# Optimization experiments

Hardware: AMD Instinct MI355X
Metric: run time of the kernel (lower is better)

The kernel has to match this reference:

```python
import jax, jax.numpy as jnp
import numpy as np

B = 4096
INPUT_DIM = 512
MAX_DIM = 4096
ACTIVE = 2048
INIT_LEAK = 0.1
INIT_THRESH = 0.5


def setup_inputs() -> dict:
    key = jax.random.key(0)
    ks = jax.random.split(key, 6)
    inputs = jax.random.normal(ks[0], (B, INPUT_DIM), dtype=jnp.float32)
    state = jax.random.normal(ks[1], (B, MAX_DIM), dtype=jnp.float32)
    # pre-allocated weights at max dimension, stddev=0.1 (RandomNormal)
    W_res = 0.1 * jax.random.normal(ks[2], (MAX_DIM, MAX_DIM), dtype=jnp.float32)
    W_in = 0.1 * jax.random.normal(ks[3], (MAX_DIM, INPUT_DIM), dtype=jnp.float32)
    W_gate = 0.1 * jax.random.normal(ks[4], (3 * MAX_DIM, INPUT_DIM), dtype=jnp.float32)
    # logit(leak_rate) and inverse-softplus(spike_threshold) constant inits
    leak_param = jnp.full((MAX_DIM,), np.log(INIT_LEAK / (1.0 - INIT_LEAK)), dtype=jnp.float32)
    thresh_param = jnp.full((MAX_DIM,), np.log(np.exp(INIT_THRESH) - 1.0), dtype=jnp.float32)
    return {
        "inputs": inputs,
        "state": state,
        "W_res": W_res,
        "W_in": W_in,
        "W_gate": W_gate,
        "leak_param": leak_param,
        "thresh_param": thresh_param,
        "active_size": ACTIVE,
    }


def reference(inputs, state, W_res, W_in, W_gate, leak_param, thresh_param, active_size):
    A = int(active_size)
    prev = state[:, :A]                              # [B, A]
    leak = jax.nn.sigmoid(leak_param[:A])            # [A]
    thresh = jax.nn.softplus(thresh_param[:A])       # [A]
    input_part = inputs @ W_in[:A].T                 # [B, A]
    res_part = prev @ W_res[:A, :A]                  # [B, A]
    gates = jax.nn.sigmoid(inputs @ W_gate[:3 * A].T)  # [B, 3A]
    i_gate, f_gate, o_gate = jnp.split(gates, 3, axis=-1)
    s = (1.0 - leak) * (f_gate * prev) + leak * jnp.tanh(i_gate * (input_part + res_part))
    s = o_gate * s
    s = jnp.where(s > thresh, s - thresh, s)         # spike-and-reset
    pad = state.shape[1] - A
    return jnp.pad(s, ((0, 0), (0, pad)))            # [B, MAX_DIM]
```

## Files before the change

### kernel.cpp

```cpp
#include <hip/hip_runtime.h>
#include <math.h>

typedef _Float16 f16;
typedef _Float16 f16x8 __attribute__((ext_vector_type(8)));
typedef _Float16 f16x4v __attribute__((ext_vector_type(4)));
typedef float f32x4 __attribute__((ext_vector_type(4)));

#define SPLIT_SC  2048.0f
#define INV_SPLIT (1.0f / 2048.0f)

__device__ __forceinline__ float sigmoidf_(float x) { return 1.0f / (1.0f + expf(-x)); }

#define GLOAD(ldsptr, gptr)                                                              \
    __builtin_amdgcn_global_load_lds((const __attribute__((address_space(1))) void*)(gptr), \
                                     (__attribute__((address_space(3))) void*)(ldsptr), 16, 0, 0)


__global__ void ksplit(const float* __restrict__ src, f16* __restrict__ dh,
                       f16* __restrict__ dl, int nquads)
{
    int i = blockIdx.x * blockDim.x + threadIdx.x;
    if (i >= nquads) return;
    float4 v = *(const float4*)(src + (size_t)i * 4);
    f16 h0 = (f16)v.x, h1 = (f16)v.y, h2 = (f16)v.z, h3 = (f16)v.w;
    f16x4v hv = {h0, h1, h2, h3};
    f16x4v lv = {(f16)((v.x - (float)h0) * SPLIT_SC), (f16)((v.y - (float)h1) * SPLIT_SC),
                 (f16)((v.z - (float)h2) * SPLIT_SC), (f16)((v.w - (float)h3) * SPLIT_SC)};
    *(f16x4v*)(dh + (size_t)i * 4) = hv;
    *(f16x4v*)(dl + (size_t)i * 4) = lv;
}

__global__ void ksplit_state(const float* __restrict__ src, f16* __restrict__ dh,
                             f16* __restrict__ dl)
{
    int idx = blockIdx.x * blockDim.x + threadIdx.x;
    int r = idx >> 9, c = (idx & 511) * 4;
    float4 v = *(const float4*)(src + (size_t)r * 4096 + c);
    f16 h0 = (f16)v.x, h1 = (f16)v.y, h2 = (f16)v.z, h3 = (f16)v.w;
    f16x4v hv = {h0, h1, h2, h3};
    f16x4v lv = {(f16)((v.x - (float)h0) * SPLIT_SC), (f16)((v.y - (float)h1) * SPLIT_SC),
                 (f16)((v.z - (float)h2) * SPLIT_SC), (f16)((v.w - (float)h3) * SPLIT_SC)};
    *(f16x4v*)(dh + (size_t)r * 2048 + c) = hv;
    *(f16x4v*)(dl + (size_t)r * 2048 + c) = lv;
}

__global__ void ktrsplit(const float* __restrict__ src, f16* __restrict__ th_,
                         f16* __restrict__ tl_)
{
    __shared__ float tile[32][33];
    const int tx = threadIdx.x & 31, ty = threadIdx.x >> 5;
    const int n0 = blockIdx.x * 32, k0 = blockIdx.y * 32;
    #pragma unroll
    for (int i = 0; i < 4; ++i)
        tile[ty + 8 * i][tx] = src[(size_t)(k0 + ty + 8 * i) * 4096 + n0 + tx];
    __syncthreads();
    #pragma unroll
    for (int i = 0; i < 4; ++i) {
        const int nl = ty + 8 * i;
        const float v = tile[tx][nl];
        const f16 h = (f16)v;
        const f16 l = (f16)((v - (float)h) * SPLIT_SC);
        const size_t o = (size_t)(n0 + nl) * 2048 + k0 + tx;
        th_[o] = h;
        tl_[o] = l;
    }
}

__global__ __launch_bounds__(256, 2)
void kgemm_res(const f16* __restrict__ Ah, const f16* __restrict__ Al,
               const f16* __restrict__ Bh, const f16* __restrict__ Bl,
               float* __restrict__ R)
{
    __shared__ __align__(16) f16 smem[4 * 4096];
    char* sbase = (char*)smem;

    const int tid = threadIdx.x;
    const int lane = tid & 63, w = tid >> 6;
    const int m0 = blockIdx.y * 128, n0 = blockIdx.x * 128;
    const int wm = (w >> 1) * 64, wn = (w & 1) * 64;
    const int lr = lane & 15, kg = lane >> 4;
    const int sw = (kg ^ ((lr >> 1) & 3)) << 4;
    const int srow = lane >> 2;
    const int sslot = (lane & 3) ^ ((lane >> 3) & 3);

    int aoff[4], boff[4];
    #pragma unroll
    for (int i = 0; i < 4; ++i) {
        aoff[i] = (wm + i * 16 + lr) * 64 + sw;
        boff[i] = (wn + i * 16 + lr) * 64 + sw;
    }

    f32x4 acc0[4][4], acc1[4][4];
    const f32x4 z4 = {0.f, 0.f, 0.f, 0.f};
    #pragma unroll
    for (int i = 0; i < 4; ++i)
        #pragma unroll
        for (int j = 0; j < 4; ++j) { acc0[i][j] = z4; acc1[i][j] = z4; }

    const int arow = m0 + 32 * w + srow;
    const int brow = n0 + 32 * w + srow;
    const f16* gAh = Ah + (size_t)arow * 2048 + sslot * 8;
    const f16* gAl = Al + (size_t)arow * 2048 + sslot * 8;
    const f16* gBh = Bh + (size_t)brow * 2048 + sslot * 8;
    const f16* gBl = Bl + (size_t)brow * 2048 + sslot * 8;
    char* lw = sbase + (32 * w) * 64;

    for (int t = 0; t < 64; ++t) {
        const int k0 = t * 32;
        #pragma unroll
        for (int i = 0; i < 2; ++i) {
            const size_t go = (size_t)i * 16 * 2048 + k0;
            GLOAD(lw + i * 1024 +     0, gAh + go);
            GLOAD(lw + i * 1024 +  8192, gAl + go);
            GLOAD(lw + i * 1024 + 16384, gBh + go);
            GLOAD(lw + i * 1024 + 24576, gBl + go);
        }
        asm volatile("s_waitcnt vmcnt(0)" ::: "memory");
        __syncthreads();

        f16x8 fah[4], fal[4], fbh[4], fbl[4];
        #pragma unroll
        for (int i = 0; i < 4; ++i) {
            fah[i] = *(const f16x8*)(sbase +         aoff[i]);
            fal[i] = *(const f16x8*)(sbase +  8192 + aoff[i]);
            fbh[i] = *(const f16x8*)(sbase + 16384 + boff[i]);
            fbl[i] = *(const f16x8*)(sbase + 24576 + boff[i]);
        }
        #pragma unroll
        for (int mi = 0; mi < 4; ++mi)
            #pragma unroll
            for (int nj = 0; nj < 4; ++nj) {
                acc0[mi][nj] = __builtin_amdgcn_mfma_f32_16x16x32_f16(fah[mi], fbh[nj], acc0[mi][nj], 0, 0, 0);
                acc1[mi][nj] = __builtin_amdgcn_mfma_f32_16x16x32_f16(fah[mi], fbl[nj], acc1[mi][nj], 0, 0, 0);
                acc1[mi][nj] = __builtin_amdgcn_mfma_f32_16x16x32_f16(fal[mi], fbh[nj], acc1[mi][nj], 0, 0, 0);
            }
        __syncthreads();
    }

    #pragma unroll
    for (int mi = 0; mi < 4; ++mi)
        #pragma unroll
        for (int nj = 0; nj < 4; ++nj) {
            const int col = n0 + wn + nj * 16 + lr;
            #pragma unroll
            for (int rg = 0; rg < 4; ++rg) {
                const int row = m0 + wm + mi * 16 + kg * 4 + rg;
                R[(size_t)row * 2048 + col] = acc0[mi][nj][rg] + acc1[mi][nj][rg] * INV_SPLIT;
            }
        }
}

__global__ __launch_bounds__(256, 2)
void kgemm_fused(const f16* __restrict__ Ah, const f16* __restrict__ Al,
                 const f16* __restrict__ Wh, const f16* __restrict__ Wl,
                 const float* __restrict__ R,
                 const float* __restrict__ state,
                 const float* __restrict__ leak_p, const float* __restrict__ th_p,
                 float* __restrict__ out)
{
    __shared__ __align__(16) f16 smem[10 * 2048];
    char* sbase = (char*)smem;

    const int tid = threadIdx.x;
    const int lane = tid & 63, w = tid >> 6;
    const int m0 = blockIdx.y * 64, n0 = blockIdx.x * 64;
    const int wm = (w >> 1) * 32, wn = (w & 1) * 32;
    const int lr = lane & 15, kg = lane >> 4;
    const int sw = (kg ^ ((lr >> 1) & 3)) << 4;
    const int srow = lane >> 2;
    const int sslot = (lane & 3) ^ ((lane >> 3) & 3);

    int aoff[2], boff[2];
    #pragma unroll
    for (int i = 0; i < 2; ++i) {
        aoff[i] = (wm + i * 16 + lr) * 64 + sw;
        boff[i] = (wn + i * 16 + lr) * 64 + sw;
    }

    f32x4 acc0[4][2][2], acc1[4][2][2];
    const f32x4 z4 = {0.f, 0.f, 0.f, 0.f};
    #pragma unroll
    for (int q = 0; q < 4; ++q)
        #pragma unroll
        for (int i = 0; i < 2; ++i)
            #pragma unroll
            for (int j = 0; j < 2; ++j) { acc0[q][i][j] = z4; acc1[q][i][j] = z4; }

    const f16* gsrc[10];
    gsrc[0] = Ah + (size_t)(m0 + 16 * w + srow) * 512 + sslot * 8;
    gsrc[1] = Al + (size_t)(m0 + 16 * w + srow) * 512 + sslot * 8;
    #pragma unroll
    for (int q = 0; q < 4; ++q) {
        const size_t brow = (size_t)(q * 2048 + n0 + 16 * w + srow) * 512 + sslot * 8;
        gsrc[2 + 2 * q] = Wh + brow;
        gsrc[3 + 2 * q] = Wl + brow;
    }

    for (int t = 0; t < 16; ++t) {
        const int k0 = t * 32;
        #pragma unroll
        for (int j = 0; j < 10; ++j)
            GLOAD(sbase + j * 4096 + w * 1024, gsrc[j] + k0);
        asm volatile("s_waitcnt vmcnt(0)" ::: "memory");
        __syncthreads();

        f16x8 fah[2], fal[2];
        #pragma unroll
        for (int i = 0; i < 2; ++i) {
            fah[i] = *(const f16x8*)(sbase +        aoff[i]);
            fal[i] = *(const f16x8*)(sbase + 4096 + aoff[i]);
        }
        #pragma unroll
        for (int q = 0; q < 4; ++q) {
            f16x8 fbh[2], fbl[2];
            #pragma unroll
            for (int j = 0; j < 2; ++j) {
                fbh[j] = *(const f16x8*)(sbase + (2 + 2 * q) * 4096 + boff[j]);
                fbl[j] = *(const f16x8*)(sbase + (3 + 2 * q) * 4096 + boff[j]);
            }
            #pragma unroll
            for (int mi = 0; mi < 2; ++mi)
                #pragma unroll
                for (int nj = 0; nj < 2; ++nj) {
                    acc0[q][mi][nj] = __builtin_amdgcn_mfma_f32_16x16x32_f16(fah[mi], fbh[nj], acc0[q][mi][nj], 0, 0, 0);
                    acc1[q][mi][nj] = __builtin_amdgcn_mfma_f32_16x16x32_f16(fah[mi], fbl[nj], acc1[q][mi][nj], 0, 0, 0);
                    acc1[q][mi][nj] = __builtin_amdgcn_mfma_f32_16x16x32_f16(fal[mi], fbh[nj], acc1[q][mi][nj], 0, 0, 0);
                }
        }
        __syncthreads();
    }

    #pragma unroll
    for (int nj = 0; nj < 2; ++nj) {
        const int n = n0 + wn + nj * 16 + lr;
        const float lk = sigmoidf_(leak_p[n]);
        const float th = log1pf(expf(th_p[n]));
        #pragma unroll
        for (int mi = 0; mi < 2; ++mi)
            #pragma unroll
            for (int rg = 0; rg < 4; ++rg) {
                const int m = m0 + wm + mi * 16 + kg * 4 + rg;
                const float ip = acc0[0][mi][nj][rg] + acc1[0][mi][nj][rg] * INV_SPLIT;
                const float gi = sigmoidf_(acc0[1][mi][nj][rg] + acc1[1][mi][nj][rg] * INV_SPLIT);
                const float gf = sigmoidf_(acc0[2][mi][nj][rg] + acc1[2][mi][nj][rg] * INV_SPLIT);
                const float go = sigmoidf_(acc0[3][mi][nj][rg] + acc1[3][mi][nj][rg] * INV_SPLIT);
                const float res = R[(size_t)m * 2048 + n];
                const float prev = state[(size_t)m * 4096 + n];
                const float x = gi * (ip + res);
                float s = (1.0f - lk) * (gf * prev) + lk * tanhf(x);
                s *= go;
                out[(size_t)m * 4096 + n] = (s > th) ? (s - th) : s;
            }
    }
}

__global__ void kzero(float* __restrict__ out) {
    const int idx = blockIdx.x * blockDim.x + threadIdx.x;
    const int r = idx >> 9, cq = idx & 511;
    *(float4*)(out + (size_t)r * 4096 + 2048 + cq * 4) = make_float4(0.f, 0.f, 0.f, 0.f);
}

extern "C" void kernel_launch(void* const* d_in, const int* in_sizes, int n_in,
                              void* d_out, int out_size, void* d_ws, size_t ws_size,
                              hipStream_t stream)
{
    const float* inputs = (const float*)d_in[0];
    const float* state  = (const float*)d_in[1];
    const float* W_res  = (const float*)d_in[2];
    const float* W_in   = (const float*)d_in[3];
    const float* W_gate = (const float*)d_in[4];
    const float* leak_p = (const float*)d_in[5];
    const float* th_p   = (const float*)d_in[6];
    float* out = (float*)d_out;

    if (ws_size < 109051904u) return;
    char* ws = (char*)d_ws;
    float* R  = (float*)(ws);
    f16* sAh  = (f16*)(ws + 33554432);
    f16* sAl  = (f16*)(ws + 50331648);
    f16* inh  = (f16*)(ws + 67108864);
    f16* inl  = (f16*)(ws + 71303168);
    f16* W1h  = (f16*)(ws + 75497472);
    f16* W1l  = (f16*)(ws + 83886080);
    f16* Bth  = (f16*)(ws + 92274688);
    f16* Btl  = (f16*)(ws + 100663296);

    kzero<<<(4096 * 2048 / 4) / 256, 256, 0, stream>>>(out);

    ksplit<<<(4096 * 512 / 4) / 256, 256, 0, stream>>>(inputs, inh, inl, 4096 * 512 / 4);
    ksplit<<<(2048 * 512 / 4) / 256, 256, 0, stream>>>(W_in, W1h, W1l, 2048 * 512 / 4);
    ksplit<<<(6144 * 512 / 4) / 256, 256, 0, stream>>>(W_gate, W1h + 1048576, W1l + 1048576,
                                                       6144 * 512 / 4);
    ksplit_state<<<(4096 * 512) / 256, 256, 0, stream>>>(state, sAh, sAl);
    ktrsplit<<<dim3(64, 64), 256, 0, stream>>>(W_res, Bth, Btl);

    kgemm_res<<<dim3(2048 / 128, 4096 / 128), 256, 0, stream>>>(sAh, sAl, Bth, Btl, R);
    kgemm_fused<<<dim3(2048 / 64, 4096 / 64), 256, 0, stream>>>(inh, inl, W1h, W1l, R, state,
                                                                leak_p, th_p, out);
}
```

Baseline: 416.6 us.

## Double-buffer GEMM LDS loads, fuse split kernels and zero-fill, vectorize transpose

Both GEMM kernels now use two LDS buffers, so the global-to-LDS loads for the next k-tile are issued before the MFMAs on the current tile run. The three input/weight split launches become one kernel, and the separate zero-padding kernel is folded into the fused GEMM epilogue. The transpose-split kernel moves to 64x64 tiles with float4 reads and 16-byte f16 writes. Doubling LDS per block may cut occupancy in kgemm_res, which now needs 64KB per block against a launch bound of 2 blocks.

```diff
diff --git a/kernel.cpp b/kernel.cpp
--- a/kernel.cpp
+++ b/kernel.cpp
@@ -16,18 +16,26 @@
                                      (__attribute__((address_space(3))) void*)(ldsptr), 16, 0, 0)
 
 
-__global__ void ksplit(const float* __restrict__ src, f16* __restrict__ dh,
-                       f16* __restrict__ dl, int nquads)
-{
-    int i = blockIdx.x * blockDim.x + threadIdx.x;
-    if (i >= nquads) return;
-    float4 v = *(const float4*)(src + (size_t)i * 4);
-    f16 h0 = (f16)v.x, h1 = (f16)v.y, h2 = (f16)v.z, h3 = (f16)v.w;
+__global__ void ksplit_all(const float* __restrict__ inputs, const float* __restrict__ W_in,
+                           const float* __restrict__ W_gate,
+                           f16* __restrict__ inh, f16* __restrict__ inl,
+                           f16* __restrict__ W1h, f16* __restrict__ W1l)
+{
+    const int i = blockIdx.x * blockDim.x + threadIdx.x;
+    const int Q_IN = 4096 * 512 / 4;
+    const int Q_WIN = 2048 * 512 / 4;
+    const float* src; f16 *dh, *dl; int q;
+    if (i < Q_IN)              { src = inputs; dh = inh; dl = inl; q = i; }
+    else if (i < Q_IN + Q_WIN) { src = W_in;  dh = W1h; dl = W1l; q = i - Q_IN; }
+    else                       { src = W_gate; dh = W1h + 1048576; dl = W1l + 1048576;
+                                 q = i - Q_IN - Q_WIN; }
+    const float4 v = *(const float4*)(src + (size_t)q * 4);
+    const f16 h0 = (f16)v.x, h1 = (f16)v.y, h2 = (f16)v.z, h3 = (f16)v.w;
     f16x4v hv = {h0, h1, h2, h3};
     f16x4v lv = {(f16)((v.x - (float)h0) * SPLIT_SC), (f16)((v.y - (float)h1) * SPLIT_SC),
                  (f16)((v.z - (float)h2) * SPLIT_SC), (f16)((v.w - (float)h3) * SPLIT_SC)};
-    *(f16x4v*)(dh + (size_t)i * 4) = hv;
-    *(f16x4v*)(dl + (size_t)i * 4) = lv;
+    *(f16x4v*)(dh + (size_t)q * 4) = hv;
+    *(f16x4v*)(dl + (size_t)q * 4) = lv;
 }
 
 __global__ void ksplit_state(const float* __restrict__ src, f16* __restrict__ dh,
@@ -47,23 +55,35 @@
 __global__ void ktrsplit(const float* __restrict__ src, f16* __restrict__ th_,
                          f16* __restrict__ tl_)
 {
-    __shared__ float tile[32][33];
-    const int tx = threadIdx.x & 31, ty = threadIdx.x >> 5;
-    const int n0 = blockIdx.x * 32, k0 = blockIdx.y * 32;
-    #pragma unroll
-    for (int i = 0; i < 4; ++i)
-        tile[ty + 8 * i][tx] = src[(size_t)(k0 + ty + 8 * i) * 4096 + n0 + tx];
+    __shared__ float tile[64][65];
+    const int tid = threadIdx.x;
+    const int n0 = blockIdx.x * 64, k0 = blockIdx.y * 64;
+    const int rr = tid >> 4, c4 = (tid & 15) * 4;
+    #pragma unroll
+    for (int i = 0; i < 4; ++i) {
+        const float4 v = *(const float4*)(src + (size_t)(k0 + rr + 16 * i) * 4096 + n0 + c4);
+        tile[rr + 16 * i][c4 + 0] = v.x;
+        tile[rr + 16 * i][c4 + 1] = v.y;
+        tile[rr + 16 * i][c4 + 2] = v.z;
+        tile[rr + 16 * i][c4 + 3] = v.w;
+    }
     __syncthreads();
-    #pragma unroll
-    for (int i = 0; i < 4; ++i) {
-        const int nl = ty + 8 * i;
-        const float v = tile[tx][nl];
-        const f16 h = (f16)v;
-        const f16 l = (f16)((v - (float)h) * SPLIT_SC);
-        const size_t o = (size_t)(n0 + nl) * 2048 + k0 + tx;
-        th_[o] = h;
-        tl_[o] = l;
-    }
+    const int nl = tid >> 2, kq = (tid & 3) * 16;
+    f16x8 h0, h1, l0, l1;
+    #pragma unroll
+    for (int j = 0; j < 8; ++j) {
+        const float va = tile[kq + j][nl];
+        const float vb = tile[kq + 8 + j][nl];
+        const f16 ha = (f16)va, hb = (f16)vb;
+        h0[j] = ha; h1[j] = hb;
+        l0[j] = (f16)((va - (float)ha) * SPLIT_SC);
+        l1[j] = (f16)((vb - (float)hb) * SPLIT_SC);
+    }
+    const size_t o = (size_t)(n0 + nl) * 2048 + k0 + kq;
+    *(f16x8*)(th_ + o)     = h0;
+    *(f16x8*)(th_ + o + 8) = h1;
+    *(f16x8*)(tl_ + o)     = l0;
+    *(f16x8*)(tl_ + o + 8) = l1;
 }
 
 __global__ __launch_bounds__(256, 2)
@@ -71,7 +91,7 @@
                const f16* __restrict__ Bh, const f16* __restrict__ Bl,
                float* __restrict__ R)
 {
-    __shared__ __align__(16) f16 smem[4 * 4096];
+    __shared__ __align__(16) f16 smem[2 * 4 * 4096];
     char* sbase = (char*)smem;
 
     const int tid = threadIdx.x;
@@ -103,28 +123,27 @@
     const f16* gAl = Al + (size_t)arow * 2048 + sslot * 8;
     const f16* gBh = Bh + (size_t)brow * 2048 + sslot * 8;
     const f16* gBl = Bl + (size_t)brow * 2048 + sslot * 8;
-    char* lw = sbase + (32 * w) * 64;
-
-    for (int t = 0; t < 64; ++t) {
-        const int k0 = t * 32;
+
+    auto stage = [&](int buf, int k0) {
+        char* lwb = sbase + buf * 32768 + (32 * w) * 64;
         #pragma unroll
         for (int i = 0; i < 2; ++i) {
-            const size_t go = (size_t)i * 16 * 2048 + k0;
-            GLOAD(lw + i * 1024 +     0, gAh + go);
-            GLOAD(lw + i * 1024 +  8192, gAl + go);
-            GLOAD(lw + i * 1024 + 16384, gBh + go);
-            GLOAD(lw + i * 1024 + 24576, gBl + go);
-        }
-        asm volatile("s_waitcnt vmcnt(0)" ::: "memory");
-        __syncthreads();
-
+            const size_t go = (size_t)(i * 16) * 2048 + k0;
+            GLOAD(lwb + i * 1024 +     0, gAh + go);
+            GLOAD(lwb + i * 1024 +  8192, gAl + go);
+            GLOAD(lwb + i * 1024 + 16384, gBh + go);
+            GLOAD(lwb + i * 1024 + 24576, gBl + go);
+        }
+    };
+    auto compute = [&](int buf) {
+        const char* sb = sbase + buf * 32768;
         f16x8 fah[4], fal[4], fbh[4], fbl[4];
         #pragma unroll
         for (int i = 0; i < 4; ++i) {
-            fah[i] = *(const f16x8*)(sbase +         aoff[i]);
-            fal[i] = *(const f16x8*)(sbase +  8192 + aoff[i]);
-            fbh[i] = *(const f16x8*)(sbase + 16384 + boff[i]);
-            fbl[i] = *(const f16x8*)(sbase + 24576 + boff[i]);
+            fah[i] = *(const f16x8*)(sb +         aoff[i]);
+            fal[i] = *(const f16x8*)(sb +  8192 + aoff[i]);
+            fbh[i] = *(const f16x8*)(sb + 16384 + boff[i]);
+            fbl[i] = *(const f16x8*)(sb + 24576 + boff[i]);
         }
         #pragma unroll
         for (int mi = 0; mi < 4; ++mi)
@@ -134,6 +153,19 @@
                 acc1[mi][nj] = __builtin_amdgcn_mfma_f32_16x16x32_f16(fah[mi], fbl[nj], acc1[mi][nj], 0, 0, 0);
                 acc1[mi][nj] = __builtin_amdgcn_mfma_f32_16x16x32_f16(fal[mi], fbh[nj], acc1[mi][nj], 0, 0, 0);
             }
+    };
+
+    stage(0, 0);
+    asm volatile("s_waitcnt vmcnt(0)" ::: "memory");
+    __syncthreads();
+    for (int t = 0; t < 64; t += 2) {
+        stage(1, (t + 1) * 32);
+        compute(0);
+        asm volatile("s_waitcnt vmcnt(0)" ::: "memory");
+        __syncthreads();
+        if (t + 2 < 64) stage(0, (t + 2) * 32);
+        compute(1);
+        asm volatile("s_waitcnt vmcnt(0)" ::: "memory");
         __syncthreads();
     }
 
@@ -158,7 +190,7 @@
                  const float* __restrict__ leak_p, const float* __restrict__ th_p,
                  float* __restrict__ out)
 {
-    __shared__ __align__(16) f16 smem[10 * 2048];
+    __shared__ __align__(16) f16 smem[2 * 10 * 2048];
     char* sbase = (char*)smem;
 
     const int tid = threadIdx.x;
@@ -196,27 +228,27 @@
         gsrc[3 + 2 * q] = Wl + brow;
     }
 
-    for (int t = 0; t < 16; ++t) {
-        const int k0 = t * 32;
+    auto stage = [&](int buf, int k0) {
+        char* lwb = sbase + buf * 40960 + w * 1024;
         #pragma unroll
         for (int j = 0; j < 10; ++j)
-            GLOAD(sbase + j * 4096 + w * 1024, gsrc[j] + k0);
-        asm volatile("s_waitcnt vmcnt(0)" ::: "memory");
-        __syncthreads();
-
+            GLOAD(lwb + j * 4096, gsrc[j] + k0);
+    };
+    auto compute = [&](int buf) {
+        const char* sb = sbase + buf * 40960;
         f16x8 fah[2], fal[2];
         #pragma unroll
         for (int i = 0; i < 2; ++i) {
-            fah[i] = *(const f16x8*)(sbase +        aoff[i]);
-            fal[i] = *(const f16x8*)(sbase + 4096 + aoff[i]);
+            fah[i] = *(const f16x8*)(sb +        aoff[i]);
+            fal[i] = *(const f16x8*)(sb + 4096 + aoff[i]);
         }
         #pragma unroll
         for (int q = 0; q < 4; ++q) {
             f16x8 fbh[2], fbl[2];
             #pragma unroll
             for (int j = 0; j < 2; ++j) {
-                fbh[j] = *(const f16x8*)(sbase + (2 + 2 * q) * 4096 + boff[j]);
-                fbl[j] = *(const f16x8*)(sbase + (3 + 2 * q) * 4096 + boff[j]);
+                fbh[j] = *(const f16x8*)(sb + (2 + 2 * q) * 4096 + boff[j]);
+                fbl[j] = *(const f16x8*)(sb + (3 + 2 * q) * 4096 + boff[j]);
             }
             #pragma unroll
             for (int mi = 0; mi < 2; ++mi)
@@ -227,6 +259,19 @@
                     acc1[q][mi][nj] = __builtin_amdgcn_mfma_f32_16x16x32_f16(fal[mi], fbh[nj], acc1[q][mi][nj], 0, 0, 0);
                 }
         }
+    };
+
+    stage(0, 0);
+    asm volatile("s_waitcnt vmcnt(0)" ::: "memory");
+    __syncthreads();
+    for (int t = 0; t < 16; t += 2) {
+        stage(1, (t + 1) * 32);
+        compute(0);
+        asm volatile("s_waitcnt vmcnt(0)" ::: "memory");
+        __syncthreads();
+        if (t + 2 < 16) stage(0, (t + 2) * 32);
+        compute(1);
+        asm volatile("s_waitcnt vmcnt(0)" ::: "memory");
         __syncthreads();
     }
 
@@ -252,12 +297,17 @@
                 out[(size_t)m * 4096 + n] = (s > th) ? (s - th) : s;
             }
     }
-}
-
-__global__ void kzero(float* __restrict__ out) {
-    const int idx = blockIdx.x * blockDim.x + threadIdx.x;
-    const int r = idx >> 9, cq = idx & 511;
-    *(float4*)(out + (size_t)r * 4096 + 2048 + cq * 4) = make_float4(0.f, 0.f, 0.f, 0.f);
+
+    {
+        const int pr = m0 + (tid >> 2);
+        const int pc = 2048 + blockIdx.x * 64 + (tid & 3) * 16;
+        float* p = out + (size_t)pr * 4096 + pc;
+        const float4 z = make_float4(0.f, 0.f, 0.f, 0.f);
+        *(float4*)(p)      = z;
+        *(float4*)(p + 4)  = z;
+        *(float4*)(p + 8)  = z;
+        *(float4*)(p + 12) = z;
+    }
 }
 
 extern "C" void kernel_launch(void* const* d_in, const int* in_sizes, int n_in,
@@ -285,14 +335,10 @@
     f16* Bth  = (f16*)(ws + 92274688);
     f16* Btl  = (f16*)(ws + 100663296);
 
-    kzero<<<(4096 * 2048 / 4) / 256, 256, 0, stream>>>(out);
-
-    ksplit<<<(4096 * 512 / 4) / 256, 256, 0, stream>>>(inputs, inh, inl, 4096 * 512 / 4);
-    ksplit<<<(2048 * 512 / 4) / 256, 256, 0, stream>>>(W_in, W1h, W1l, 2048 * 512 / 4);
-    ksplit<<<(6144 * 512 / 4) / 256, 256, 0, stream>>>(W_gate, W1h + 1048576, W1l + 1048576,
-                                                       6144 * 512 / 4);
     ksplit_state<<<(4096 * 512) / 256, 256, 0, stream>>>(state, sAh, sAl);
-    ktrsplit<<<dim3(64, 64), 256, 0, stream>>>(W_res, Bth, Btl);
+    ktrsplit<<<dim3(32, 32), 256, 0, stream>>>(W_res, Bth, Btl);
+    ksplit_all<<<(4096 * 512 / 4 + 2048 * 512 / 4 + 6144 * 512 / 4) / 256, 256, 0, stream>>>(
+        inputs, W_in, W_gate, inh, inl, W1h, W1l);
 
     kgemm_res<<<dim3(2048 / 128, 4096 / 128), 256, 0, stream>>>(sAh, sAl, Bth, Btl, R);
     kgemm_fused<<<dim3(2048 / 64, 4096 / 64), 256, 0, stream>>>(inh, inl, W1h, W1l, R, state,
```

Result: no change. 415.0 us (-0.4%).
